# Performance work log

Measured on AMD Instinct MI355X. Metric: run time of the kernel, lower is better.

Reference implementation:

```python
import jax, jax.numpy as jnp
import numpy as np


def setup_inputs() -> dict:
    key = jax.random.key(0)
    ks = jax.random.split(key, 5)
    B, S, D = 8, 2048, 1024  # batch, seq_len, d_query == d_value
    return {
        "query": jax.random.normal(ks[0], (B, S, D), dtype=jnp.float32),
        "key": jax.random.normal(ks[1], (B, S, D), dtype=jnp.float32),
        "value": jax.random.normal(ks[2], (B, S, D), dtype=jnp.float32),
        "cell_mask": jnp.ones((B, S, S), dtype=jnp.float32),
        "seq_mask": jnp.ones((B, S), dtype=jnp.float32),
        "W_k": jax.random.normal(ks[3], (D, D), dtype=jnp.float32) * (1.0 / np.sqrt(D)),
        "b_k": jnp.zeros((D,), dtype=jnp.float32),
        "W_o": jax.random.normal(ks[4], (D, D), dtype=jnp.float32) * (1.0 / np.sqrt(D)),
        "b_o": jnp.zeros((D,), dtype=jnp.float32),
    }


def reference(query, key, value, cell_mask, seq_mask, W_k, b_k, W_o, b_o):
    # k_proj = linear_layer(key): torch Linear uses x @ W.T + b
    k_proj = jnp.einsum("bkd,qd->bkq", key, W_k) + b_k  # (B, S, d_query)
    scores = jnp.einsum("bqd,bkd->bqk", query, k_proj)  # (B, Sq, Sk)
    # additive log-mask bias: log(cell_mask) + log(seq_mask broadcast over query dim)
    scores = scores + jnp.log(cell_mask) + jnp.log(seq_mask)[:, None, :]
    p_attn = jax.nn.softmax(scores, axis=-1)
    x = jnp.einsum("bqk,bkd->bqd", p_attn, value)  # (B, Sq, d_value)
    return jnp.einsum("bqd,od->bqo", x, W_o) + b_o
```

## Files before the change

kernel.cpp:

```cpp
#include <hip/hip_runtime.h>
#include <stdint.h>

typedef __attribute__((ext_vector_type(8))) __bf16 bf16x8;
typedef __attribute__((ext_vector_type(4))) float f32x4;

#define DEVI __device__ __forceinline__

DEVI unsigned short f2bf(float f) {
  unsigned u = __builtin_bit_cast(unsigned, f);
  u += 0x7fffu + ((u >> 16) & 1u);
  return (unsigned short)(u >> 16);
}
DEVI float bf2f(unsigned short h) {
  unsigned u = ((unsigned)h) << 16;
  return __builtin_bit_cast(float, u);
}

DEVI void gload_lds16(const unsigned short* g, unsigned char* lds) {
  __builtin_amdgcn_global_load_lds(
      (const __attribute__((address_space(1))) void*)g,
      (__attribute__((address_space(3))) void*)lds, 16, 0, 0);
}

__global__ __launch_bounds__(256) void split_kernel(
    const float* __restrict__ x, unsigned short* __restrict__ hi,
    unsigned short* __restrict__ lo, int nvec) {
  long long i = (long long)blockIdx.x * 256 + threadIdx.x;
  if (i >= nvec) return;
  float4 f = reinterpret_cast<const float4*>(x)[i];
  ushort4 h, l;
  h.x = f2bf(f.x); l.x = f2bf(f.x - bf2f(h.x));
  h.y = f2bf(f.y); l.y = f2bf(f.y - bf2f(h.y));
  h.z = f2bf(f.z); l.z = f2bf(f.z - bf2f(h.z));
  h.w = f2bf(f.w); l.w = f2bf(f.w - bf2f(h.w));
  reinterpret_cast<ushort4*>(hi)[i] = h;
  reinterpret_cast<ushort4*>(lo)[i] = l;
}

__global__ __launch_bounds__(256) void cast_kernel(
    const float* __restrict__ x, unsigned short* __restrict__ hi, int nvec) {
  long long i = (long long)blockIdx.x * 256 + threadIdx.x;
  if (i >= nvec) return;
  float4 f = reinterpret_cast<const float4*>(x)[i];
  ushort4 h;
  h.x = f2bf(f.x); h.y = f2bf(f.y); h.z = f2bf(f.z); h.w = f2bf(f.w);
  reinterpret_cast<ushort4*>(hi)[i] = h;
}

__global__ __launch_bounds__(256) void transpose_cast_kernel(
    const float* __restrict__ v, unsigned short* __restrict__ vT, int S, int D) {
  __shared__ float tile[32][33];
  const int tx = threadIdx.x, ty = threadIdx.y;
  const int k0 = blockIdx.x * 32, d0 = blockIdx.y * 32, b = blockIdx.z;
  const float* vb = v + (long long)b * S * D;
  unsigned short* vTb = vT + (long long)b * S * D;
#pragma unroll
  for (int j = 0; j < 4; ++j) {
    int kl = ty + j * 8;
    tile[kl][tx] = vb[(long long)(k0 + kl) * D + d0 + tx];
  }
  __syncthreads();
#pragma unroll
  for (int j = 0; j < 4; ++j) {
    int dl = ty + j * 8;
    vTb[(long long)(d0 + dl) * S + k0 + tx] = f2bf(tile[tx][dl]);
  }
}

DEVI float wred_max(float x) {
#pragma unroll
  for (int o = 32; o > 0; o >>= 1) x = fmaxf(x, __shfl_xor(x, o));
  return x;
}
DEVI float wred_sum(float x) {
#pragma unroll
  for (int o = 32; o > 0; o >>= 1) x += __shfl_xor(x, o);
  return x;
}

__global__ __launch_bounds__(256) void softmax_kernel(
    const float* __restrict__ scores, const float* __restrict__ cell,
    const float* __restrict__ seq, unsigned short* __restrict__ p, int S) {
  const long long row = blockIdx.x;
  const int b = (int)(row / S);
  const long long base = row * S;
  const int t = threadIdx.x, lane = t & 63, wid = t >> 6;
  __shared__ float red[8];

  const float4* sc = (const float4*)(scores + base);
  const float4* cm = (const float4*)(cell + base);
  const float4* sm = (const float4*)(seq + (long long)b * S);

  float4 x0 = sc[2 * t], x1 = sc[2 * t + 1];
  float4 c0 = cm[2 * t], c1 = cm[2 * t + 1];
  float4 q0 = sm[2 * t], q1 = sm[2 * t + 1];
  float v[8];
  v[0] = x0.x + __logf(c0.x) + __logf(q0.x);
  v[1] = x0.y + __logf(c0.y) + __logf(q0.y);
  v[2] = x0.z + __logf(c0.z) + __logf(q0.z);
  v[3] = x0.w + __logf(c0.w) + __logf(q0.w);
  v[4] = x1.x + __logf(c1.x) + __logf(q1.x);
  v[5] = x1.y + __logf(c1.y) + __logf(q1.y);
  v[6] = x1.z + __logf(c1.z) + __logf(q1.z);
  v[7] = x1.w + __logf(c1.w) + __logf(q1.w);

  float m = v[0];
#pragma unroll
  for (int j = 1; j < 8; ++j) m = fmaxf(m, v[j]);
  m = wred_max(m);
  if (lane == 0) red[wid] = m;
  __syncthreads();
  m = fmaxf(fmaxf(red[0], red[1]), fmaxf(red[2], red[3]));

  float e[8], s = 0.f;
#pragma unroll
  for (int j = 0; j < 8; ++j) { e[j] = __expf(v[j] - m); s += e[j]; }
  s = wred_sum(s);
  if (lane == 0) red[4 + wid] = s;
  __syncthreads();
  s = red[4] + red[5] + red[6] + red[7];
  const float inv = 1.0f / s;

  uint4 o;
  o.x = (unsigned)f2bf(e[0] * inv) | ((unsigned)f2bf(e[1] * inv) << 16);
  o.y = (unsigned)f2bf(e[2] * inv) | ((unsigned)f2bf(e[3] * inv) << 16);
  o.z = (unsigned)f2bf(e[4] * inv) | ((unsigned)f2bf(e[5] * inv) << 16);
  o.w = (unsigned)f2bf(e[6] * inv) | ((unsigned)f2bf(e[7] * inv) << 16);
  ((uint4*)(p + base))[t] = o;
}

template <int SPLIT, int OUTMODE, bool BIAS>
__global__ __launch_bounds__(256, 2) void gemm_bt(
    const unsigned short* __restrict__ Ah, const unsigned short* __restrict__ Al,
    const unsigned short* __restrict__ Bh, const unsigned short* __restrict__ Bl,
    float* __restrict__ Cf, unsigned short* __restrict__ Chi,
    unsigned short* __restrict__ Clo, const float* __restrict__ bias,
    int M, int N, int K, long long sA, long long sB, long long sC) {
  constexpr int BK = (SPLIT == 3) ? 32 : 64;
  constexpr int TILEB = 128 * BK * 2;
  constexpr int NT = (SPLIT == 3) ? 4 : 2;
  __shared__ __align__(16) unsigned char smem[2 * NT * TILEB];

  const int tid = threadIdx.x, lane = tid & 63, wid = tid >> 6;
  const int wm = wid >> 1, wn = wid & 1;
  const int r16 = lane & 15, q4 = lane >> 4;
  const int bn0 = blockIdx.x * 128, bm0 = blockIdx.y * 128;
  const int bz = blockIdx.z;

  Ah += (long long)bz * sA;
  Bh += (long long)bz * sB;
  if (SPLIT == 3) { Al += (long long)bz * sA; Bl += (long long)bz * sB; }
  const long long cb = (long long)bz * sC;

  auto stage = [&](int buf, int kt) {
    const int k0 = kt * BK;
    if (SPLIT == 3) {
      const unsigned short* src = (wid == 0) ? Ah : (wid == 1) ? Al : (wid == 2) ? Bh : Bl;
      const int row0 = (wid < 2) ? bm0 : bn0;
      unsigned char* dst = smem + (size_t)(buf * 4 + wid) * TILEB;
#pragma unroll
      for (int i = 0; i < 8; ++i) {
        const int row = i * 16 + (lane >> 2);
        const int sg = (lane & 3) ^ ((row >> 1) & 3);
        gload_lds16(src + (long long)(row0 + row) * K + k0 + sg * 8, dst + i * 1024);
      }
    } else {
      const unsigned short* src = (wid < 2) ? Ah : Bh;
      const int row0 = (wid < 2) ? bm0 : bn0;
      const int half = wid & 1;
      unsigned char* dst = smem + (size_t)(buf * 2 + (wid >> 1)) * TILEB + half * 8192;
#pragma unroll
      for (int i = 0; i < 8; ++i) {
        const int row = half * 64 + i * 8 + (lane >> 3);
        const int sg = (lane & 7) ^ (row & 7);
        gload_lds16(src + (long long)(row0 + row) * K + k0 + sg * 8, dst + i * 1024);
      }
    }
  };

  auto foff = [&](int r, int ks) -> int {
    return (BK == 64) ? (r * 128 + ((((ks << 2) + q4) ^ (r & 7)) << 4))
                      : (r * 64 + ((q4 ^ ((r >> 1) & 3)) << 4));
  };

  f32x4 acc[4][4];
#pragma unroll
  for (int mi = 0; mi < 4; ++mi)
#pragma unroll
    for (int ni = 0; ni < 4; ++ni) acc[mi][ni] = (f32x4){0.f, 0.f, 0.f, 0.f};

  const int nk = K / BK;
  int buf = 0;
  stage(0, 0);
  for (int kt = 0; kt < nk; ++kt) {
    __syncthreads();
    if (kt + 1 < nk) stage(buf ^ 1, kt + 1);
    const unsigned char* tA = smem + (size_t)((SPLIT == 3) ? (buf * 4 + 0) : (buf * 2 + 0)) * TILEB;
    const unsigned char* tB = smem + (size_t)((SPLIT == 3) ? (buf * 4 + 2) : (buf * 2 + 1)) * TILEB;
    const unsigned char* tAl = (SPLIT == 3) ? smem + (size_t)(buf * 4 + 1) * TILEB : nullptr;
    const unsigned char* tBl = (SPLIT == 3) ? smem + (size_t)(buf * 4 + 3) * TILEB : nullptr;
#pragma unroll
    for (int ks = 0; ks < BK / 32; ++ks) {
      bf16x8 a_h[4], b_h[4], a_l[4], b_l[4];
#pragma unroll
      for (int mi = 0; mi < 4; ++mi) {
        const int r = wm * 64 + mi * 16 + r16;
        const int off = foff(r, ks);
        a_h[mi] = *(const bf16x8*)(tA + off);
        if (SPLIT == 3) a_l[mi] = *(const bf16x8*)(tAl + off);
      }
#pragma unroll
      for (int ni = 0; ni < 4; ++ni) {
        const int r = wn * 64 + ni * 16 + r16;
        const int off = foff(r, ks);
        b_h[ni] = *(const bf16x8*)(tB + off);
        if (SPLIT == 3) b_l[ni] = *(const bf16x8*)(tBl + off);
      }
#pragma unroll
      for (int mi = 0; mi < 4; ++mi)
#pragma unroll
        for (int ni = 0; ni < 4; ++ni) {
          acc[mi][ni] = __builtin_amdgcn_mfma_f32_16x16x32_bf16(a_h[mi], b_h[ni], acc[mi][ni], 0, 0, 0);
          if (SPLIT == 3) {
            acc[mi][ni] = __builtin_amdgcn_mfma_f32_16x16x32_bf16(a_h[mi], b_l[ni], acc[mi][ni], 0, 0, 0);
            acc[mi][ni] = __builtin_amdgcn_mfma_f32_16x16x32_bf16(a_l[mi], b_h[ni], acc[mi][ni], 0, 0, 0);
          }
        }
    }
    buf ^= 1;
  }

#pragma unroll
  for (int mi = 0; mi < 4; ++mi) {
#pragma unroll
    for (int ni = 0; ni < 4; ++ni) {
      const int col = bn0 + wn * 64 + ni * 16 + r16;
      const float bv = BIAS ? bias[col] : 0.0f;
#pragma unroll
      for (int j = 0; j < 4; ++j) {
        const int row = bm0 + wm * 64 + mi * 16 + q4 * 4 + j;
        const float cv = acc[mi][ni][j] + bv;
        const long long idx = cb + (long long)row * N + col;
        if (OUTMODE == 0) {
          Cf[idx] = cv;
        } else if (OUTMODE == 1) {
          Chi[idx] = f2bf(cv);
        } else {
          unsigned short h = f2bf(cv);
          Chi[idx] = h;
          Clo[idx] = f2bf(cv - bf2f(h));
        }
      }
    }
  }
}

extern "C" void kernel_launch(void* const* d_in, const int* in_sizes, int n_in,
                              void* d_out, int out_size, void* d_ws, size_t ws_size,
                              hipStream_t stream) {
  const float* query = (const float*)d_in[0];
  const float* key   = (const float*)d_in[1];
  const float* value = (const float*)d_in[2];
  const float* cell  = (const float*)d_in[3];
  const float* seq   = (const float*)d_in[4];
  const float* W_k   = (const float*)d_in[5];
  const float* b_k   = (const float*)d_in[6];
  const float* W_o   = (const float*)d_in[7];
  const float* b_o   = (const float*)d_in[8];
  float* out = (float*)d_out;

  const int B = 8, S = 2048, D = 1024;
  const long long NE = (long long)B * S * D;
  const long long NS = (long long)B * S * S;

  unsigned char* ws = (unsigned char*)d_ws;
  size_t off = 0;
  auto alloc = [&](size_t bytes) -> unsigned char* {
    unsigned char* pp = ws + off;
    off += (bytes + 255) & ~(size_t)255;
    return pp;
  };
  unsigned short* qhi  = (unsigned short*)alloc(NE * 2);
  unsigned short* qlo  = (unsigned short*)alloc(NE * 2);
  unsigned short* kphi = (unsigned short*)alloc(NE * 2);
  unsigned short* kplo = (unsigned short*)alloc(NE * 2);
  unsigned short* vT   = (unsigned short*)alloc(NE * 2);
  unsigned short* khi  = (unsigned short*)alloc(NE * 2);
  unsigned short* klo  = (unsigned short*)alloc(NE * 2);
  float*          scores = (float*)alloc(NS * 4);
  unsigned short* wkhi = (unsigned short*)alloc((size_t)D * D * 2);
  unsigned short* wklo = (unsigned short*)alloc((size_t)D * D * 2);
  unsigned short* wo   = (unsigned short*)alloc((size_t)D * D * 2);
  unsigned short* p    = khi;
  unsigned short* xbf  = (unsigned short*)scores;
  (void)ws_size; (void)in_sizes; (void)n_in; (void)out_size;

  split_kernel<<<dim3(NE / 1024), 256, 0, stream>>>(query, qhi, qlo, (int)(NE / 4));
  split_kernel<<<dim3(NE / 1024), 256, 0, stream>>>(key, khi, klo, (int)(NE / 4));
  split_kernel<<<dim3(D * D / 1024), 256, 0, stream>>>(W_k, wkhi, wklo, D * D / 4);
  cast_kernel<<<dim3(D * D / 1024), 256, 0, stream>>>(W_o, wo, D * D / 4);
  transpose_cast_kernel<<<dim3(S / 32, D / 32, B), dim3(32, 8), 0, stream>>>(value, vT, S, D);

  gemm_bt<3, 2, true><<<dim3(D / 128, (B * S) / 128, 1), 256, 0, stream>>>(
      khi, klo, wkhi, wklo, nullptr, kphi, kplo, b_k, B * S, D, D, 0, 0, 0);

  gemm_bt<3, 0, false><<<dim3(S / 128, S / 128, B), 256, 0, stream>>>(
      qhi, qlo, kphi, kplo, scores, nullptr, nullptr, nullptr, S, S, D,
      (long long)S * D, (long long)S * D, (long long)S * S);

  softmax_kernel<<<dim3(B * S), 256, 0, stream>>>(scores, cell, seq, p, S);

  gemm_bt<1, 1, false><<<dim3(D / 128, S / 128, B), 256, 0, stream>>>(
      p, nullptr, vT, nullptr, nullptr, xbf, nullptr, nullptr, S, D, S,
      (long long)S * S, (long long)S * D, (long long)S * D);

  gemm_bt<1, 0, true><<<dim3(D / 128, (B * S) / 128, 1), 256, 0, stream>>>(
      xbf, nullptr, wo, nullptr, out, nullptr, nullptr, b_o, B * S, D, D, 0, 0, 0);
}
```

Baseline: 840.8 us.

## Add 256x256-tile 512-thread GEMM with phased LDS pipeline for split-bf16 GEMMs

Adds a new GEMM kernel with 256x256 output tiles, 8 waves and 128KB of dynamic LDS. Global-to-LDS copies are interleaved across four compute phases per k-step, with barriers, setprio and sched_barrier around the MFMA blocks. The kernel replaces the 128x128 kernel for the two 3-pass split-bf16 GEMMs (key projection and QK^T) to raise data reuse per LDS load and overlap loads with compute. The larger tiles give fewer blocks and higher register pressure, and 128KB of LDS may limit occupancy to one block per CU.

After: 811.9 us. -3.4%, faster.

```diff
diff --git a/kernel.cpp b/kernel.cpp
--- a/kernel.cpp
+++ b/kernel.cpp
@@ -21,6 +21,14 @@
       (const __attribute__((address_space(1))) void*)g,
       (__attribute__((address_space(3))) void*)lds, 16, 0, 0);
 }
+
+#define MEMFENCE asm volatile("" ::: "memory")
+#define BARRIER()                      \
+  do {                                 \
+    MEMFENCE;                          \
+    __builtin_amdgcn_s_barrier();      \
+    MEMFENCE;                          \
+  } while (0)
 
 __global__ __launch_bounds__(256) void split_kernel(
     const float* __restrict__ x, unsigned short* __restrict__ hi,
@@ -127,6 +135,172 @@
   o.z = (unsigned)f2bf(e[4] * inv) | ((unsigned)f2bf(e[5] * inv) << 16);
   o.w = (unsigned)f2bf(e[6] * inv) | ((unsigned)f2bf(e[7] * inv) << 16);
   ((uint4*)(p + base))[t] = o;
+}
+
+template <int SPLIT, int OUTMODE, bool BIAS>
+__global__ __launch_bounds__(512, 2) void gemm256(
+    const unsigned short* __restrict__ Ah, const unsigned short* __restrict__ Al,
+    const unsigned short* __restrict__ Bh, const unsigned short* __restrict__ Bl,
+    float* __restrict__ Cf, unsigned short* __restrict__ Chi,
+    unsigned short* __restrict__ Clo, const float* __restrict__ bias,
+    int M, int N, int K, long long sA, long long sB, long long sC) {
+  constexpr int BK = (SPLIT == 3) ? 32 : 64;
+  extern __shared__ unsigned char smem[];
+
+  const int tid = threadIdx.x, lane = tid & 63, wid = tid >> 6;
+  const int wm = wid >> 2, wn = wid & 3;
+  const int r16 = lane & 15, q4 = lane >> 4;
+  const int bn0 = blockIdx.x * 256, bm0 = blockIdx.y * 256;
+  const int bz = blockIdx.z;
+
+  Ah += (long long)bz * sA;
+  Bh += (long long)bz * sB;
+  if (SPLIT == 3) { Al += (long long)bz * sA; Bl += (long long)bz * sB; }
+  const long long cbase = (long long)bz * sC;
+  const int nk = K / BK;
+
+  auto stageg = [&](int h) {
+    const int ts = h >> 2, j = h & 3;
+    const int k0 = ts * BK;
+    unsigned char* slotb = smem + (ts & 1) * 65536;
+    if constexpr (SPLIT == 3) {
+      const unsigned short* src = (j == 0) ? Ah : (j == 1) ? Al : (j == 2) ? Bh : Bl;
+      const int row0 = (j < 2) ? bm0 : bn0;
+#pragma unroll
+      for (int i = 0; i < 2; ++i) {
+        const int seg = i * 8 + wid;
+        const int row = seg * 16 + (lane >> 2);
+        const int c = (lane & 3) ^ ((row >> 1) & 3);
+        gload_lds16(src + (long long)(row0 + row) * K + k0 + c * 8,
+                    slotb + j * 16384 + seg * 1024);
+      }
+    } else {
+      const unsigned short* src = (j < 2) ? Ah : Bh;
+      const int row0 = (j < 2) ? bm0 : bn0;
+#pragma unroll
+      for (int i = 0; i < 2; ++i) {
+        const int seg = i * 8 + wid;
+        const int row = (j & 1) * 128 + seg * 8 + (lane >> 3);
+        const int c = (lane & 7) ^ (row & 7);
+        gload_lds16(src + (long long)(row0 + row) * K + k0 + c * 8,
+                    slotb + (j >> 1) * 32768 + (j & 1) * 16384 + seg * 1024);
+      }
+    }
+  };
+
+  f32x4 acc[8][4];
+#pragma unroll
+  for (int mi = 0; mi < 8; ++mi)
+#pragma unroll
+    for (int ni = 0; ni < 4; ++ni) acc[mi][ni] = (f32x4){0.f, 0.f, 0.f, 0.f};
+
+  bf16x8 a_h[4], a_l[4], b_h[2], b_l[2];
+
+  stageg(0); stageg(1); stageg(2); stageg(3); stageg(4);
+  asm volatile("s_waitcnt vmcnt(2)" ::: "memory");
+  BARRIER();
+
+  for (int tau = 0; tau < nk; ++tau) {
+    const unsigned char* sb = smem + (tau & 1) * 65536;
+    const int hb = 4 * tau + 5;
+
+    auto LOADA = [&](int rb) {
+#pragma unroll
+      for (int mq = 0; mq < 4; ++mq) {
+        const int r = wm * 128 + rb * 64 + mq * 16 + r16;
+        if constexpr (SPLIT == 3) {
+          const int o = r * 64 + ((q4 ^ ((r >> 1) & 3)) << 4);
+          a_h[mq] = *(const bf16x8*)(sb + o);
+          a_l[mq] = *(const bf16x8*)(sb + 16384 + o);
+        } else {
+          a_h[mq] = *(const bf16x8*)(sb + r * 128 + ((q4 ^ (r & 7)) << 4));
+          a_l[mq] = *(const bf16x8*)(sb + r * 128 + (((4 + q4) ^ (r & 7)) << 4));
+        }
+      }
+    };
+    auto LOADB = [&](int cb) {
+#pragma unroll
+      for (int nq = 0; nq < 2; ++nq) {
+        const int r = wn * 64 + cb * 32 + nq * 16 + r16;
+        if constexpr (SPLIT == 3) {
+          const int o = r * 64 + ((q4 ^ ((r >> 1) & 3)) << 4);
+          b_h[nq] = *(const bf16x8*)(sb + 32768 + o);
+          b_l[nq] = *(const bf16x8*)(sb + 49152 + o);
+        } else {
+          b_h[nq] = *(const bf16x8*)(sb + 32768 + r * 128 + ((q4 ^ (r & 7)) << 4));
+          b_l[nq] = *(const bf16x8*)(sb + 32768 + r * 128 + (((4 + q4) ^ (r & 7)) << 4));
+        }
+      }
+    };
+    auto MMA = [&](int rb, int cb) {
+#pragma unroll
+      for (int mq = 0; mq < 4; ++mq)
+#pragma unroll
+        for (int nq = 0; nq < 2; ++nq) {
+          f32x4& A = acc[rb * 4 + mq][cb * 2 + nq];
+          A = __builtin_amdgcn_mfma_f32_16x16x32_bf16(a_h[mq], b_h[nq], A, 0, 0, 0);
+          if constexpr (SPLIT == 3) {
+            A = __builtin_amdgcn_mfma_f32_16x16x32_bf16(a_h[mq], b_l[nq], A, 0, 0, 0);
+            A = __builtin_amdgcn_mfma_f32_16x16x32_bf16(a_l[mq], b_h[nq], A, 0, 0, 0);
+          } else {
+            A = __builtin_amdgcn_mfma_f32_16x16x32_bf16(a_l[mq], b_l[nq], A, 0, 0, 0);
+          }
+        }
+    };
+
+#define PHASE_MID(RB, CB)                      \
+  BARRIER();                                   \
+  asm volatile("s_waitcnt lgkmcnt(0)" ::: "memory"); \
+  __builtin_amdgcn_sched_barrier(0);           \
+  __builtin_amdgcn_s_setprio(1);               \
+  MMA(RB, CB);                                 \
+  __builtin_amdgcn_s_setprio(0);               \
+  __builtin_amdgcn_sched_barrier(0);           \
+  BARRIER()
+
+    LOADA(0); LOADB(0);
+    if (hb + 0 < 4 * nk) stageg(hb + 0);
+    PHASE_MID(0, 0);
+    LOADB(1);
+    if (hb + 1 < 4 * nk) stageg(hb + 1);
+    PHASE_MID(0, 1);
+    LOADA(1);
+    if (hb + 2 < 4 * nk) stageg(hb + 2);
+    PHASE_MID(1, 1);
+    LOADB(0);
+    if (hb + 3 < 4 * nk) {
+      stageg(hb + 3);
+      asm volatile("s_waitcnt vmcnt(2)" ::: "memory");
+    } else {
+      asm volatile("s_waitcnt vmcnt(0)" ::: "memory");
+    }
+    PHASE_MID(1, 0);
+#undef PHASE_MID
+  }
+
+#pragma unroll
+  for (int mi = 0; mi < 8; ++mi) {
+#pragma unroll
+    for (int ni = 0; ni < 4; ++ni) {
+      const int col = bn0 + wn * 64 + ni * 16 + r16;
+      const float bv = BIAS ? bias[col] : 0.0f;
+#pragma unroll
+      for (int j = 0; j < 4; ++j) {
+        const int row = bm0 + wm * 128 + mi * 16 + q4 * 4 + j;
+        const float cv = acc[mi][ni][j] + bv;
+        const long long idx = cbase + (long long)row * N + col;
+        if (OUTMODE == 0) {
+          Cf[idx] = cv;
+        } else if (OUTMODE == 1) {
+          Chi[idx] = f2bf(cv);
+        } else {
+          unsigned short h = f2bf(cv);
+          Chi[idx] = h;
+          Clo[idx] = f2bf(cv - bf2f(h));
+        }
+      }
+    }
+  }
 }
 
 template <int SPLIT, int OUTMODE, bool BIAS>
@@ -295,16 +469,21 @@
   unsigned short* xbf  = (unsigned short*)scores;
   (void)ws_size; (void)in_sizes; (void)n_in; (void)out_size;
 
+  (void)hipFuncSetAttribute(reinterpret_cast<const void*>(gemm256<3, 2, true>),
+                            hipFuncAttributeMaxDynamicSharedMemorySize, 131072);
+  (void)hipFuncSetAttribute(reinterpret_cast<const void*>(gemm256<3, 0, false>),
+                            hipFuncAttributeMaxDynamicSharedMemorySize, 131072);
+
   split_kernel<<<dim3(NE / 1024), 256, 0, stream>>>(query, qhi, qlo, (int)(NE / 4));
   split_kernel<<<dim3(NE / 1024), 256, 0, stream>>>(key, khi, klo, (int)(NE / 4));
   split_kernel<<<dim3(D * D / 1024), 256, 0, stream>>>(W_k, wkhi, wklo, D * D / 4);
   cast_kernel<<<dim3(D * D / 1024), 256, 0, stream>>>(W_o, wo, D * D / 4);
   transpose_cast_kernel<<<dim3(S / 32, D / 32, B), dim3(32, 8), 0, stream>>>(value, vT, S, D);
 
-  gemm_bt<3, 2, true><<<dim3(D / 128, (B * S) / 128, 1), 256, 0, stream>>>(
+  gemm256<3, 2, true><<<dim3(D / 256, (B * S) / 256, 1), 512, 131072, stream>>>(
       khi, klo, wkhi, wklo, nullptr, kphi, kplo, b_k, B * S, D, D, 0, 0, 0);
 
-  gemm_bt<3, 0, false><<<dim3(S / 128, S / 128, B), 256, 0, stream>>>(
+  gemm256<3, 0, false><<<dim3(S / 256, S / 256, B), 512, 131072, stream>>>(
       qhi, qlo, kphi, kplo, scores, nullptr, nullptr, nullptr, S, S, D,
       (long long)S * D, (long long)S * D, (long long)S * S);
 
```
